# Kernel tuning notes

Hardware: AMD Instinct MI355X
Metric: run time of the kernel (lower is better)

## Reference

```python
import jax, jax.numpy as jnp
import numpy as np

D_MODEL = 1024
D_FF = 4096
N_EXPERTS = 8
TOP_K = 2
BATCH = 4
SEQ = 2048


def setup_inputs() -> dict:
    key = jax.random.key(0)
    k0, k1, k2, k3, k4 = jax.random.split(key, 5)
    x = jax.random.normal(k0, (BATCH, SEQ, D_MODEL), dtype=jnp.float32)
    # MLP router: Linear(d,d) + bias, Tanh, Linear(d,E) no bias
    Wg1 = jax.random.normal(k1, (D_MODEL, D_MODEL), dtype=jnp.float32) * (1.0 / np.sqrt(D_MODEL))
    bg1 = jnp.zeros((D_MODEL,), dtype=jnp.float32)
    Wg2 = jax.random.normal(k2, (D_MODEL, N_EXPERTS), dtype=jnp.float32) * (1.0 / np.sqrt(D_MODEL))
    # ParallelExperts weights: [E, in, out] (bias=False)
    W1 = jax.random.normal(k3, (N_EXPERTS, D_MODEL, D_FF), dtype=jnp.float32) * 0.02
    W2 = jax.random.normal(k4, (N_EXPERTS, D_FF, D_MODEL), dtype=jnp.float32) * 0.02
    return {"x": x, "Wg1": Wg1, "bg1": bg1, "Wg2": Wg2, "W1": W1, "W2": W2}


def reference(x, Wg1, bg1, Wg2, W1, W2):
    B, L, d = x.shape
    T = B * L
    xf = x.reshape(T, d)

    # ---- top-k gating (eval mode: no noise, no dropout, no skip_mask) ----
    logits = jnp.tanh(xf @ Wg1 + bg1) @ Wg2          # [T, E]
    probs = jax.nn.softmax(logits, axis=-1)          # [T, E]
    top_k_gates, top_k_idx = jax.lax.top_k(probs, TOP_K)
    top_k_gates = top_k_gates / (top_k_gates.sum(axis=-1, keepdims=True) + 1e-6)
    # dense gate matrix: gates[t, e] = normalized gate if e selected for token t else 0
    gates = jnp.zeros_like(probs).at[jnp.arange(T)[:, None], top_k_idx].set(top_k_gates)

    # ---- expert FFNs + gate-weighted combine ----
    # Mathematically identical to scatter-dispatch/grouped-GEMM/index_add combine:
    # y_t = sum_e gates[t,e] * (gelu(x_t @ W1_e) @ W2_e); unselected experts have gate 0.
    # Scan over the small fixed expert axis to avoid an [E, T, d_ff] intermediate.
    def body(y, scanned):
        w1, w2, g = scanned                           # [d,h], [h,d], [T]
        h = jax.nn.gelu(xf @ w1)                      # [T, h]
        return y + (h @ w2) * g[:, None], None

    y0 = jnp.zeros((T, d), dtype=x.dtype)
    y, _ = jax.lax.scan(body, y0, (W1, W2, gates.T))

    # all aux-loss coefficients default to 0 -> loss is 0
    loss = jnp.asarray(0.0, dtype=x.dtype)
    return y.reshape(B, L, d), loss
```

## Files before the change

kernel.cpp:

```cpp
#include <hip/hip_runtime.h>
#include <hip/hip_bf16.h>
#include <math.h>

#define T_TOK 8192
#define DM 1024
#define DFF 4096
#define NE 8
#define HROWS 16512
#define MAX_TILES 136
#define TPX 17

typedef __attribute__((ext_vector_type(8))) short bf16x8;
typedef __attribute__((ext_vector_type(4))) float f32x4;
typedef __attribute__((ext_vector_type(8))) _Float16 f16x8;
typedef __attribute__((ext_vector_type(4))) _Float16 f16x4;

__device__ __forceinline__ void async16(const void* g, void* l) {
  __builtin_amdgcn_global_load_lds((const __attribute__((address_space(1))) void*)g,
                                   (__attribute__((address_space(3))) void*)l, 16, 0, 0);
}

__device__ __forceinline__ unsigned short f2b(float f) {
  __hip_bfloat16 h = __float2bfloat16(f);
  return *reinterpret_cast<unsigned short*>(&h);
}

__device__ __forceinline__ float tanh_fast(float z) {
  return 1.f - 2.f / (__expf(2.f * z) + 1.f);
}

__device__ __forceinline__ float gelu_fast(float v) {
  float u = v + 0.044715f * v * v * v;
  return v / (1.f + __expf(-1.5957691216057308f * u));
}

__global__ void split_x_kernel(const float* __restrict__ in, unsigned short* __restrict__ xb,
                               _Float16* __restrict__ xh, _Float16* __restrict__ xl) {
  int i = blockIdx.x * blockDim.x + threadIdx.x;
  float4 v = reinterpret_cast<const float4*>(in)[i];
  ushort4 ob;
  f16x4 oh, ol;
  float f, hf;
  f = v.x; oh[0] = (_Float16)f; hf = (float)oh[0]; ol[0] = (_Float16)((f - hf) * 2048.0f); ob.x = f2b(f);
  f = v.y; oh[1] = (_Float16)f; hf = (float)oh[1]; ol[1] = (_Float16)((f - hf) * 2048.0f); ob.y = f2b(f);
  f = v.z; oh[2] = (_Float16)f; hf = (float)oh[2]; ol[2] = (_Float16)((f - hf) * 2048.0f); ob.z = f2b(f);
  f = v.w; oh[3] = (_Float16)f; hf = (float)oh[3]; ol[3] = (_Float16)((f - hf) * 2048.0f); ob.w = f2b(f);
  reinterpret_cast<ushort4*>(xb)[i] = ob;
  reinterpret_cast<f16x4*>(xh)[i] = oh;
  reinterpret_cast<f16x4*>(xl)[i] = ol;
}

__global__ void transpose_split_w_kernel(const float* __restrict__ in,
                                         _Float16* __restrict__ outh, _Float16* __restrict__ outl) {
  __shared__ float tile[32][33];
  int r0 = blockIdx.y * 32, c0 = blockIdx.x * 32;
  int tx = threadIdx.x, ty = threadIdx.y;
#pragma unroll
  for (int i = 0; i < 32; i += 8) tile[ty + i][tx] = in[(size_t)(r0 + ty + i) * DM + c0 + tx];
  __syncthreads();
#pragma unroll
  for (int i = 0; i < 32; i += 8) {
    float f = tile[tx][ty + i];
    _Float16 h = (_Float16)f;
    size_t idx = (size_t)(c0 + ty + i) * DM + r0 + tx;
    outh[idx] = h;
    outl[idx] = (_Float16)((f - (float)h) * 2048.0f);
  }
}

__global__ void transpose_cast_kernel(const float* __restrict__ in, unsigned short* __restrict__ out,
                                      int R, int C) {
  __shared__ float tile[32][33];
  int e = blockIdx.z;
  int r0 = blockIdx.y * 32, c0 = blockIdx.x * 32;
  const float* src = in + (size_t)e * R * C;
  unsigned short* dst = out + (size_t)e * R * C;
  int tx = threadIdx.x, ty = threadIdx.y;
#pragma unroll
  for (int i = 0; i < 32; i += 8) tile[ty + i][tx] = src[(size_t)(r0 + ty + i) * C + c0 + tx];
  __syncthreads();
#pragma unroll
  for (int i = 0; i < 32; i += 8) dst[(size_t)(c0 + ty + i) * R + r0 + tx] = f2b(tile[tx][ty + i]);
}

__global__ __launch_bounds__(256) void router_mfma_kernel(
    const _Float16* __restrict__ xh, const _Float16* __restrict__ xl,
    const _Float16* __restrict__ wth, const _Float16* __restrict__ wtl,
    const float* __restrict__ bg1, const float* __restrict__ Wg2,
    float* __restrict__ logits) {
  __shared__ __align__(16) char AB[2][32768];
  __shared__ float lgt[128 * 2 * NE];

  const int tid = threadIdx.x;
  const int lane = tid & 63;
  const int w = tid >> 6;
  const int n0 = blockIdx.x * 128, m0 = blockIdx.y * 128;

  const int r0 = w * 16 + (lane >> 2);
  const int r1 = r0 + 64;
  const int sp = lane & 3;
  const int k0s = (sp ^ ((r0 >> 1) & 3)) * 8;
  const int k1s = (sp ^ ((r1 >> 1) & 3)) * 8;

  const _Float16* gAh0 = xh + (size_t)(m0 + r0) * DM + k0s;
  const _Float16* gAh1 = xh + (size_t)(m0 + r1) * DM + k1s;
  const _Float16* gAl0 = xl + (size_t)(m0 + r0) * DM + k0s;
  const _Float16* gAl1 = xl + (size_t)(m0 + r1) * DM + k1s;
  const _Float16* gBh0 = wth + (size_t)(n0 + r0) * DM + k0s;
  const _Float16* gBh1 = wth + (size_t)(n0 + r1) * DM + k1s;
  const _Float16* gBl0 = wtl + (size_t)(n0 + r0) * DM + k0s;
  const _Float16* gBl1 = wtl + (size_t)(n0 + r1) * DM + k1s;

  const int wr = (w >> 1) * 64, wc = (w & 1) * 64;
  const int l15 = lane & 15, ls = lane >> 4;

  f32x4 zero = {0.f, 0.f, 0.f, 0.f};
  f32x4 acc_hh[4][4], acc_c[4][4];
#pragma unroll
  for (int i = 0; i < 4; i++)
#pragma unroll
    for (int j = 0; j < 4; j++) { acc_hh[i][j] = zero; acc_c[i][j] = zero; }

  auto stage = [&](int buf, int kt) {
    char* b = &AB[buf][0] + w * 1024;
    async16(gAh0 + kt, b);
    async16(gAh1 + kt, b + 4096);
    async16(gAl0 + kt, b + 8192);
    async16(gAl1 + kt, b + 8192 + 4096);
    async16(gBh0 + kt, b + 16384);
    async16(gBh1 + kt, b + 16384 + 4096);
    async16(gBl0 + kt, b + 24576);
    async16(gBl1 + kt, b + 24576 + 4096);
  };
  auto computeTile = [&](int cur) {
    const char* base = &AB[cur][0];
    f16x8 ah[4], bh[4], tmp[4];
#pragma unroll
    for (int i = 0; i < 4; i++) {
      int ar = wr + i * 16 + l15;
      ah[i] = *(const f16x8*)(base + ar * 64 + ((ls ^ ((ar >> 1) & 3)) << 4));
    }
#pragma unroll
    for (int j = 0; j < 4; j++) {
      int br = wc + j * 16 + l15;
      bh[j] = *(const f16x8*)(base + 16384 + br * 64 + ((ls ^ ((br >> 1) & 3)) << 4));
    }
#pragma unroll
    for (int i = 0; i < 4; i++)
#pragma unroll
      for (int j = 0; j < 4; j++)
        acc_hh[i][j] = __builtin_amdgcn_mfma_f32_16x16x32_f16(ah[i], bh[j], acc_hh[i][j], 0, 0, 0);
#pragma unroll
    for (int j = 0; j < 4; j++) {
      int br = wc + j * 16 + l15;
      tmp[j] = *(const f16x8*)(base + 24576 + br * 64 + ((ls ^ ((br >> 1) & 3)) << 4));
    }
#pragma unroll
    for (int i = 0; i < 4; i++)
#pragma unroll
      for (int j = 0; j < 4; j++)
        acc_c[i][j] = __builtin_amdgcn_mfma_f32_16x16x32_f16(ah[i], tmp[j], acc_c[i][j], 0, 0, 0);
#pragma unroll
    for (int i = 0; i < 4; i++) {
      int ar = wr + i * 16 + l15;
      tmp[i] = *(const f16x8*)(base + 8192 + ar * 64 + ((ls ^ ((ar >> 1) & 3)) << 4));
    }
#pragma unroll
    for (int i = 0; i < 4; i++)
#pragma unroll
      for (int j = 0; j < 4; j++)
        acc_c[i][j] = __builtin_amdgcn_mfma_f32_16x16x32_f16(tmp[i], bh[j], acc_c[i][j], 0, 0, 0);
  };

  const int NIT = DM / 32;
  stage(0, 0);
  __syncthreads();
#pragma unroll 2
  for (int t = 0; t < NIT - 1; t++) {
    const int cur = t & 1;
    stage(cur ^ 1, (t + 1) * 32);
    computeTile(cur);
    __syncthreads();
  }
  computeTile((NIT - 1) & 1);

  float w2r[4][8];
  float bias[4];
#pragma unroll
  for (int j = 0; j < 4; j++) {
    int gn = n0 + wc + j * 16 + l15;
    bias[j] = bg1[gn];
    float4 u = *(const float4*)(Wg2 + (size_t)gn * NE);
    float4 v = *(const float4*)(Wg2 + (size_t)gn * NE + 4);
    w2r[j][0] = u.x; w2r[j][1] = u.y; w2r[j][2] = u.z; w2r[j][3] = u.w;
    w2r[j][4] = v.x; w2r[j][5] = v.y; w2r[j][6] = v.z; w2r[j][7] = v.w;
  }
  const float inv2k = 1.0f / 2048.0f;
  const int half = wc >> 6;
  const bool b3 = (l15 & 8) != 0, b2 = (l15 & 4) != 0, b1 = (l15 & 2) != 0;
#pragma unroll
  for (int i = 0; i < 4; i++) {
#pragma unroll
    for (int r = 0; r < 4; r++) {
      float s[8] = {0.f, 0.f, 0.f, 0.f, 0.f, 0.f, 0.f, 0.f};
#pragma unroll
      for (int j = 0; j < 4; j++) {
        float hv = tanh_fast(acc_hh[i][j][r] + acc_c[i][j][r] * inv2k + bias[j]);
#pragma unroll
        for (int e = 0; e < NE; e++) s[e] = fmaf(hv, w2r[j][e], s[e]);
      }
      float t4_[4], t2_[2], t1_;
#pragma unroll
      for (int q = 0; q < 4; q++) {
        float snd = b3 ? s[q] : s[q + 4];
        float rcv = __shfl_xor(snd, 8);
        t4_[q] = (b3 ? s[q + 4] : s[q]) + rcv;
      }
#pragma unroll
      for (int q = 0; q < 2; q++) {
        float snd = b2 ? t4_[q] : t4_[q + 2];
        float rcv = __shfl_xor(snd, 4);
        t2_[q] = (b2 ? t4_[q + 2] : t4_[q]) + rcv;
      }
      {
        float snd = b1 ? t2_[0] : t2_[1];
        float rcv = __shfl_xor(snd, 2);
        t1_ = (b1 ? t2_[1] : t2_[0]) + rcv;
      }
      t1_ += __shfl_xor(t1_, 1);
      int m = wr + i * 16 + ls * 4 + r;
      if (!(l15 & 1)) lgt[m * (2 * NE) + half * NE + (l15 >> 1)] = t1_;
    }
  }
  __syncthreads();
#pragma unroll
  for (int q = 0; q < 4; q++) {
    int idx = tid * 4 + q;
    int m = idx >> 3, e = idx & 7;
    float v = lgt[m * (2 * NE) + e] + lgt[m * (2 * NE) + NE + e];
    atomicAdd(&logits[(size_t)(m0 + m) * NE + e], v);
  }
}

__global__ __launch_bounds__(256) void topk_small_kernel(
    const float* __restrict__ logits, int* __restrict__ tIdx, float* __restrict__ tGate,
    int* __restrict__ counts) {
  __shared__ int lc[NE];
  const int tid = threadIdx.x;
  if (tid < NE) lc[tid] = 0;
  __syncthreads();
  int t = blockIdx.x * 256 + tid;
  float p[NE];
  float4 p0 = *(const float4*)(logits + (size_t)t * NE);
  float4 p1 = *(const float4*)(logits + (size_t)t * NE + 4);
  p[0] = p0.x; p[1] = p0.y; p[2] = p0.z; p[3] = p0.w;
  p[4] = p1.x; p[5] = p1.y; p[6] = p1.z; p[7] = p1.w;
  float v1 = -1e30f, v2 = -1e30f; int i1 = 0, i2 = 1;
#pragma unroll
  for (int e = 0; e < NE; e++) {
    float v = p[e];
    if (v > v1) { v2 = v1; i2 = i1; v1 = v; i1 = e; }
    else if (v > v2) { v2 = v; i2 = e; }
  }
  float mx = v1;
  float s = 0.f;
#pragma unroll
  for (int e = 0; e < NE; e++) s += __expf(p[e] - mx);
  float inv = 1.f / s;
  float g1 = __expf(p[i1] - mx) * inv;
  float g2 = __expf(p[i2] - mx) * inv;
  float den = 1.f / (g1 + g2 + 1e-6f);
  tIdx[2 * t] = i1; tIdx[2 * t + 1] = i2;
  tGate[2 * t] = g1 * den; tGate[2 * t + 1] = g2 * den;
  atomicAdd(&lc[i1], 1);
  atomicAdd(&lc[i2], 1);
  __syncthreads();
  if (tid < NE) atomicAdd(&counts[tid], lc[tid]);
}

__global__ void build_tiles_kernel(const int* __restrict__ counts, int* __restrict__ offsets,
                                   int4* __restrict__ desc, int* __restrict__ nTiles) {
  if (threadIdx.x != 0 || blockIdx.x != 0) return;
  int off = 0, nt = 0;
  for (int e = 0; e < NE; e++) {
    offsets[e] = off;
    int c = counts[e];
    if (c < 0) c = 0;
    if (c > 2 * T_TOK) c = 2 * T_TOK;
    for (int r = 0; r < c && nt < MAX_TILES; r += 128) {
      int v = c - r; if (v > 128) v = 128;
      desc[nt++] = make_int4(e, off + r, v, 0);
    }
    off += c;
    if (off > 2 * T_TOK) off = 2 * T_TOK;
  }
  offsets[NE] = off;
  *nTiles = nt;
}

__global__ void scatter_kernel(const int* __restrict__ tIdx, const float* __restrict__ tGate,
                               const int* __restrict__ offsets, int* __restrict__ fill,
                               int* __restrict__ tokList, float* __restrict__ gateList) {
  int id = blockIdx.x * blockDim.x + threadIdx.x;
  if (id >= 2 * T_TOK) return;
  int e = tIdx[id] & 7;
  int pos = atomicAdd(&fill[e], 1);
  int row = offsets[e] + pos;
  if (row < 0 || row >= 2 * T_TOK) return;
  tokList[row] = id >> 1;
  gateList[row] = tGate[id];
}

__global__ __launch_bounds__(256) void ffn1_kernel(
    const unsigned short* __restrict__ xb, const unsigned short* __restrict__ w1t,
    const int* __restrict__ tokList, const int4* __restrict__ desc,
    const int* __restrict__ nTiles, unsigned short* __restrict__ h) {
  const int g = blockIdx.x;
  const int tileIdx = (g & 7) * TPX + ((g >> 3) % TPX);
  const int nb = g / (8 * TPX);
  if (tileIdx >= *nTiles) return;
  int4 d = desc[tileIdx];
  const int e = d.x, rowStart = d.y, valid = d.z;
  const int n0 = nb * 128;

  __shared__ __align__(16) char AB[2][16384];

  const int tid = threadIdx.x;
  const int lane = tid & 63;
  const int w = tid >> 6;

  const int r0 = w * 16 + (lane >> 2);
  const int r1 = r0 + 64;
  const int sp = lane & 3;
  const int k0s = (sp ^ ((r0 >> 1) & 3)) * 8;
  const int k1s = (sp ^ ((r1 >> 1) & 3)) * 8;

  const unsigned short* gA0 = xb + (size_t)(tokList[rowStart + r0] & (T_TOK - 1)) * DM + k0s;
  const unsigned short* gA1 = xb + (size_t)(tokList[rowStart + r1] & (T_TOK - 1)) * DM + k1s;
  const unsigned short* gB0 = w1t + ((size_t)e * DFF + n0 + r0) * DM + k0s;
  const unsigned short* gB1 = w1t + ((size_t)e * DFF + n0 + r1) * DM + k1s;

  const int wr = (w >> 1) * 64, wc = (w & 1) * 64;
  const int l15 = lane & 15, ls = lane >> 4;

  f32x4 zero = {0.f, 0.f, 0.f, 0.f};
  f32x4 acc[4][4];
#pragma unroll
  for (int i = 0; i < 4; i++)
#pragma unroll
    for (int j = 0; j < 4; j++) acc[i][j] = zero;

  auto stage = [&](int buf, int kt) {
    char* dA = &AB[buf][0] + w * 1024;
    char* dB = dA + 8192;
    async16(gA0 + kt, dA);
    async16(gA1 + kt, dA + 4096);
    async16(gB0 + kt, dB);
    async16(gB1 + kt, dB + 4096);
  };
  auto computeTile = [&](int cur) {
    const char* rA = &AB[cur][0];
    const char* rB = rA + 8192;
    bf16x8 af[4], bfv[4];
#pragma unroll
    for (int i = 0; i < 4; i++) {
      int ar = wr + i * 16 + l15;
      af[i] = *(const bf16x8*)(rA + ar * 64 + ((ls ^ ((ar >> 1) & 3)) << 4));
    }
#pragma unroll
    for (int j = 0; j < 4; j++) {
      int br = wc + j * 16 + l15;
      bfv[j] = *(const bf16x8*)(rB + br * 64 + ((ls ^ ((br >> 1) & 3)) << 4));
    }
#pragma unroll
    for (int i = 0; i < 4; i++)
#pragma unroll
      for (int j = 0; j < 4; j++)
        acc[i][j] = __builtin_amdgcn_mfma_f32_16x16x32_bf16(af[i], bfv[j], acc[i][j], 0, 0, 0);
  };

  const int NIT = DM / 32;
  stage(0, 0);
  __syncthreads();
#pragma unroll 2
  for (int t = 0; t < NIT - 1; t++) {
    const int cur = t & 1;
    stage(cur ^ 1, (t + 1) * 32);
    computeTile(cur);
    __syncthreads();
  }
  computeTile((NIT - 1) & 1);

#pragma unroll
  for (int i = 0; i < 4; i++) {
#pragma unroll
    for (int r = 0; r < 4; r++) {
      int m = wr + i * 16 + ls * 4 + r;
      if (m < valid) {
        size_t base = (size_t)(rowStart + m) * DFF + n0 + wc;
#pragma unroll
        for (int j = 0; j < 4; j++) {
          h[base + j * 16 + l15] = f2b(gelu_fast(acc[i][j][r]));
        }
      }
    }
  }
}

__global__ __launch_bounds__(256) void ffn2_kernel(
    const unsigned short* __restrict__ h, const unsigned short* __restrict__ w2t,
    const int* __restrict__ tokList, const float* __restrict__ gateList,
    const int4* __restrict__ desc, const int* __restrict__ nTiles,
    float* __restrict__ y) {
  const int g = blockIdx.x;
  const int tileIdx = (g & 7) * TPX + ((g >> 3) % TPX);
  const int nb = g / (8 * TPX);
  if (tileIdx >= *nTiles) return;
  int4 d = desc[tileIdx];
  const int e = d.x, rowStart = d.y, valid = d.z;
  const int n0 = nb * 128;

  __shared__ __align__(16) char AB[2][16384];

  const int tid = threadIdx.x;
  const int lane = tid & 63;
  const int w = tid >> 6;

  const int r0 = w * 16 + (lane >> 2);
  const int r1 = r0 + 64;
  const int sp = lane & 3;
  const int k0s = (sp ^ ((r0 >> 1) & 3)) * 8;
  const int k1s = (sp ^ ((r1 >> 1) & 3)) * 8;

  const unsigned short* gA0 = h + (size_t)(rowStart + r0) * DFF + k0s;
  const unsigned short* gA1 = h + (size_t)(rowStart + r1) * DFF + k1s;
  const unsigned short* gB0 = w2t + ((size_t)e * DM + n0 + r0) * DFF + k0s;
  const unsigned short* gB1 = w2t + ((size_t)e * DM + n0 + r1) * DFF + k1s;

  const int wr = (w >> 1) * 64, wc = (w & 1) * 64;
  const int l15 = lane & 15, ls = lane >> 4;

  f32x4 zero = {0.f, 0.f, 0.f, 0.f};
  f32x4 acc[4][4];
#pragma unroll
  for (int i = 0; i < 4; i++)
#pragma unroll
    for (int j = 0; j < 4; j++) acc[i][j] = zero;

  auto stage = [&](int buf, int kt) {
    char* dA = &AB[buf][0] + w * 1024;
    char* dB = dA + 8192;
    async16(gA0 + kt, dA);
    async16(gA1 + kt, dA + 4096);
    async16(gB0 + kt, dB);
    async16(gB1 + kt, dB + 4096);
  };
  auto computeTile = [&](int cur) {
    const char* rA = &AB[cur][0];
    const char* rB = rA + 8192;
    bf16x8 af[4], bfv[4];
#pragma unroll
    for (int i = 0; i < 4; i++) {
      int ar = wr + i * 16 + l15;
      af[i] = *(const bf16x8*)(rA + ar * 64 + ((ls ^ ((ar >> 1) & 3)) << 4));
    }
#pragma unroll
    for (int j = 0; j < 4; j++) {
      int br = wc + j * 16 + l15;
      bfv[j] = *(const bf16x8*)(rB + br * 64 + ((ls ^ ((br >> 1) & 3)) << 4));
    }
#pragma unroll
    for (int i = 0; i < 4; i++)
#pragma unroll
      for (int j = 0; j < 4; j++)
        acc[i][j] = __builtin_amdgcn_mfma_f32_16x16x32_bf16(af[i], bfv[j], acc[i][j], 0, 0, 0);
  };

  const int NIT = DFF / 32;
  stage(0, 0);
  __syncthreads();
#pragma unroll 2
  for (int t = 0; t < NIT - 1; t++) {
    const int cur = t & 1;
    stage(cur ^ 1, (t + 1) * 32);
    computeTile(cur);
    __syncthreads();
  }
  computeTile((NIT - 1) & 1);

#pragma unroll
  for (int i = 0; i < 4; i++) {
#pragma unroll
    for (int r = 0; r < 4; r++) {
      int m = wr + i * 16 + ls * 4 + r;
      if (m < valid) {
        int row = rowStart + m;
        int tok = tokList[row] & (T_TOK - 1);
        float g2 = gateList[row];
        float* yr = y + (size_t)tok * DM + n0 + wc;
#pragma unroll
        for (int j = 0; j < 4; j++) {
          atomicAdd(&yr[j * 16 + l15], g2 * acc[i][j][r]);
        }
      }
    }
  }
}

extern "C" void kernel_launch(void* const* d_in, const int* in_sizes, int n_in,
                              void* d_out, int out_size, void* d_ws, size_t ws_size,
                              hipStream_t stream) {
  const float* x   = (const float*)d_in[0];
  const float* Wg1 = (const float*)d_in[1];
  const float* bg1 = (const float*)d_in[2];
  const float* Wg2 = (const float*)d_in[3];
  const float* W1  = (const float*)d_in[4];
  const float* W2  = (const float*)d_in[5];
  float* y = (float*)d_out;
  char* ws = (char*)d_ws;

  const size_t SZ_W1T = (size_t)NE * DFF * DM * 2;
  const size_t OFF_W1T = 0;
  const size_t OFF_W2T = OFF_W1T + SZ_W1T;
  const size_t OFF_XB  = OFF_W2T + SZ_W1T;
  const size_t OFF_H   = OFF_XB + (size_t)T_TOK * DM * 2;
  const size_t OFF_TOK = OFF_H + (size_t)HROWS * DFF * 2;
  const size_t OFF_GATE = OFF_TOK + (size_t)HROWS * 4;
  const size_t OFF_TIDX = OFF_GATE + (size_t)HROWS * 4;
  const size_t OFF_TG   = OFF_TIDX + (size_t)2 * T_TOK * 4;
  const size_t OFF_LOG  = OFF_TG + (size_t)2 * T_TOK * 4;
  const size_t OFF_META = OFF_LOG + (size_t)T_TOK * NE * 4;
  const size_t NEED = OFF_META + 4096;

  const size_t OFF_XH  = OFF_H;
  const size_t OFF_XL  = OFF_XH + (size_t)T_TOK * DM * 2;
  const size_t OFF_WTH = OFF_XL + (size_t)T_TOK * DM * 2;
  const size_t OFF_WTL = OFF_WTH + (size_t)DM * DM * 2;

  hipMemsetAsync(d_out, 0, (size_t)out_size * 4, stream);
  if (ws_size < NEED) return;

  unsigned short* w1t = (unsigned short*)(ws + OFF_W1T);
  unsigned short* w2t = (unsigned short*)(ws + OFF_W2T);
  unsigned short* xb  = (unsigned short*)(ws + OFF_XB);
  unsigned short* h   = (unsigned short*)(ws + OFF_H);
  _Float16* xh        = (_Float16*)(ws + OFF_XH);
  _Float16* xl        = (_Float16*)(ws + OFF_XL);
  _Float16* wth       = (_Float16*)(ws + OFF_WTH);
  _Float16* wtl       = (_Float16*)(ws + OFF_WTL);
  int* tokList        = (int*)(ws + OFF_TOK);
  float* gateList     = (float*)(ws + OFF_GATE);
  int* tIdx           = (int*)(ws + OFF_TIDX);
  float* tGate        = (float*)(ws + OFF_TG);
  float* logits       = (float*)(ws + OFF_LOG);
  int* counts         = (int*)(ws + OFF_META);
  int* fill           = (int*)(ws + OFF_META + 32);
  int* offsets        = (int*)(ws + OFF_META + 64);
  int* nTiles         = (int*)(ws + OFF_META + 128);
  int4* desc          = (int4*)(ws + OFF_META + 160);

  hipMemsetAsync(ws + OFF_TOK, 0, (size_t)2 * HROWS * 4, stream);
  hipMemsetAsync(ws + OFF_LOG, 0, (size_t)T_TOK * NE * 4, stream);
  hipMemsetAsync(ws + OFF_META, 0, 64, stream);

  split_x_kernel<<<dim3((T_TOK * DM / 4) / 256), dim3(256), 0, stream>>>(x, xb, xh, xl);
  transpose_split_w_kernel<<<dim3(DM / 32, DM / 32), dim3(32, 8), 0, stream>>>(Wg1, wth, wtl);
  transpose_cast_kernel<<<dim3(DFF / 32, DM / 32, NE), dim3(32, 8), 0, stream>>>(W1, w1t, DM, DFF);
  transpose_cast_kernel<<<dim3(DM / 32, DFF / 32, NE), dim3(32, 8), 0, stream>>>(W2, w2t, DFF, DM);

  router_mfma_kernel<<<dim3(DM / 128, T_TOK / 128), dim3(256), 0, stream>>>(xh, xl, wth, wtl,
                                                                            bg1, Wg2, logits);
  topk_small_kernel<<<dim3(T_TOK / 256), dim3(256), 0, stream>>>(logits, tIdx, tGate, counts);
  build_tiles_kernel<<<dim3(1), dim3(64), 0, stream>>>(counts, offsets, desc, nTiles);
  scatter_kernel<<<dim3((2 * T_TOK) / 256), dim3(256), 0, stream>>>(tIdx, tGate, offsets, fill,
                                                                    tokList, gateList);

  ffn1_kernel<<<dim3((DFF / 128) * MAX_TILES), dim3(256), 0, stream>>>(xb, w1t, tokList, desc,
                                                                       nTiles, h);
  ffn2_kernel<<<dim3((DM / 128) * MAX_TILES), dim3(256), 0, stream>>>(h, w2t, tokList, gateList,
                                                                      desc, nTiles, y);
}
```

Measured before the change: 781.7 us.

## Triple-buffer LDS staging in expert GEMMs with partial vmcnt waits

```diff
diff --git a/kernel.cpp b/kernel.cpp
--- a/kernel.cpp
+++ b/kernel.cpp
@@ -323,7 +323,7 @@
   const int e = d.x, rowStart = d.y, valid = d.z;
   const int n0 = nb * 128;
 
-  __shared__ __align__(16) char AB[2][16384];
+  __shared__ __align__(16) char AB[3][16384];
 
   const int tid = threadIdx.x;
   const int lane = tid & 63;
@@ -381,15 +381,20 @@
 
   const int NIT = DM / 32;
   stage(0, 0);
-  __syncthreads();
-#pragma unroll 2
-  for (int t = 0; t < NIT - 1; t++) {
-    const int cur = t & 1;
-    stage(cur ^ 1, (t + 1) * 32);
+  stage(1, 32);
+  int cur = 0, stg = 2;
+  for (int t = 0; t < NIT; t++) {
+    if (t < NIT - 1) asm volatile("s_waitcnt vmcnt(4)" ::: "memory");
+    else             asm volatile("s_waitcnt vmcnt(0)" ::: "memory");
+    __builtin_amdgcn_s_barrier();
+    __builtin_amdgcn_sched_barrier(0);
+    if (t < NIT - 2) {
+      stage(stg, (t + 2) * 32);
+      stg = (stg == 2) ? 0 : stg + 1;
+    }
     computeTile(cur);
-    __syncthreads();
-  }
-  computeTile((NIT - 1) & 1);
+    cur = (cur == 2) ? 0 : cur + 1;
+  }
 
 #pragma unroll
   for (int i = 0; i < 4; i++) {
@@ -420,7 +425,7 @@
   const int e = d.x, rowStart = d.y, valid = d.z;
   const int n0 = nb * 128;
 
-  __shared__ __align__(16) char AB[2][16384];
+  __shared__ __align__(16) char AB[3][16384];
 
   const int tid = threadIdx.x;
   const int lane = tid & 63;
@@ -478,15 +483,20 @@
 
   const int NIT = DFF / 32;
   stage(0, 0);
-  __syncthreads();
-#pragma unroll 2
-  for (int t = 0; t < NIT - 1; t++) {
-    const int cur = t & 1;
-    stage(cur ^ 1, (t + 1) * 32);
+  stage(1, 32);
+  int cur = 0, stg = 2;
+  for (int t = 0; t < NIT; t++) {
+    if (t < NIT - 1) asm volatile("s_waitcnt vmcnt(4)" ::: "memory");
+    else             asm volatile("s_waitcnt vmcnt(0)" ::: "memory");
+    __builtin_amdgcn_s_barrier();
+    __builtin_amdgcn_sched_barrier(0);
+    if (t < NIT - 2) {
+      stage(stg, (t + 2) * 32);
+      stg = (stg == 2) ? 0 : stg + 1;
+    }
     computeTile(cur);
-    __syncthreads();
-  }
-  computeTile((NIT - 1) & 1);
+    cur = (cur == 2) ? 0 : cur + 1;
+  }
 
 #pragma unroll
   for (int i = 0; i < 4; i++) {
```

Result: faster. 710.2 us (-9.2%).
